# Performance work log

Measured on AMD Instinct MI355X. Metric: run time of the kernel, lower is better.

The kernel has to match this reference:

```python
import jax, jax.numpy as jnp
import numpy as np

N, E, G = 100000, 1600000, 64
IN, H, OUT = 128, 64, 16  # hidden/2 = 32
SLOPE = 0.01


def setup_inputs() -> dict:
    key = jax.random.key(0)
    ks = jax.random.split(key, 7)
    features = jax.random.normal(ks[0], (N, IN), dtype=jnp.float32)
    src = jax.random.randint(ks[1], (E,), 0, N)
    dst = jax.random.randint(ks[2], (E,), 0, N)
    graph_ids = jnp.sort(jax.random.randint(ks[3], (N,), 0, G))
    # kaiming-uniform-ish fan_in init, bias=False everywhere
    W1 = jax.random.uniform(ks[4], (IN, H), jnp.float32, -1.0, 1.0) * np.sqrt(3.0 / IN)
    W2 = jax.random.uniform(ks[5], (H, H // 2), jnp.float32, -1.0, 1.0) * np.sqrt(3.0 / H)
    Wc = jax.random.uniform(ks[6], (H // 2, OUT), jnp.float32, -1.0, 1.0) * np.sqrt(3.0 / (H // 2))
    return {"features": features, "src": src, "dst": dst, "graph_ids": graph_ids,
            "W1": W1, "W2": W2, "Wc": Wc}


def _graph_conv(x, W, src, dst, n):
    # DGL GraphConv, norm='both', bias=False:
    # out = D_in^{-1/2} A (D_out^{-1/2} x) W   (degrees clamped to >= 1)
    ones = jnp.ones(src.shape[0], dtype=x.dtype)
    outdeg = jnp.clip(jax.ops.segment_sum(ones, src, num_segments=n), 1.0)
    indeg = jnp.clip(jax.ops.segment_sum(ones, dst, num_segments=n), 1.0)
    h = (x * jax.lax.rsqrt(outdeg)[:, None]) @ W  # project first (in_dim > out_dim)
    m = jax.ops.segment_sum(h[src], dst, num_segments=n)  # sparse aggregation
    return m * jax.lax.rsqrt(indeg)[:, None]


def reference(features, src, dst, graph_ids, W1, W2, Wc):
    h = jax.nn.leaky_relu(_graph_conv(features, W1, src, dst, N), SLOPE)
    h = jax.nn.leaky_relu(_graph_conv(h, W2, src, dst, N), SLOPE)
    # dropout is identity at inference
    sums = jax.ops.segment_sum(h, graph_ids, num_segments=G)
    cnts = jnp.clip(jax.ops.segment_sum(jnp.ones((N,), h.dtype), graph_ids, num_segments=G), 1.0)
    mean = sums / cnts[:, None]  # dgl.mean_nodes
    return mean @ Wc  # [G, OUT]
```

## Files before the change

kernel.cpp:

```cpp
#include <hip/hip_runtime.h>

#define NN 100000
#define NE 1600000
#define NG 64
#define D_IN 128
#define D_H 64
#define D_H2 32
#define D_OUT 16
#define SLOPE 0.01f
#define REC 48

#define BSH 9
#define NBK 196
#define NCB 256
#define CHE (NE / NCB)
#define CNT_M (2 * NBK * NCB)

typedef _Float16 half2v __attribute__((ext_vector_type(2)));
typedef _Float16 h8 __attribute__((ext_vector_type(8)));
typedef float f32x4 __attribute__((ext_vector_type(4)));

__global__ __launch_bounds__(256) void p1_count(const int* __restrict__ src,
                                                const int* __restrict__ dst,
                                                int* __restrict__ cnt) {
  __shared__ int hD[NBK], hS[NBK];
  int b = blockIdx.x, t = threadIdx.x;
  for (int i = t; i < NBK; i += 256) { hD[i] = 0; hS[i] = 0; }
  __syncthreads();
  int base = b * CHE;
  for (int i = t; i < CHE; i += 256) {
    atomicAdd(&hD[dst[base + i] >> BSH], 1);
    atomicAdd(&hS[src[base + i] >> BSH], 1);
  }
  __syncthreads();
  for (int i = t; i < NBK; i += 256) {
    cnt[i * NCB + b] = hD[i];
    cnt[(NBK + i) * NCB + b] = hS[i];
  }
}

__global__ __launch_bounds__(256) void s1_reduce(const int* __restrict__ cnt,
                                                 int* __restrict__ part) {
  __shared__ int red[256];
  int b = blockIdx.x, t = threadIdx.x;
  red[t] = cnt[b * 256 + t];
  __syncthreads();
  for (int off = 128; off > 0; off >>= 1) {
    if (t < off) red[t] += red[t + off];
    __syncthreads();
  }
  if (t == 0) part[b] = red[0];
}

__global__ __launch_bounds__(512) void s2_scan(int* __restrict__ part) {
  __shared__ int a[512], b2[512];
  int t = threadIdx.x;
  const int M = CNT_M / 256;
  int v = (t < M) ? part[t] : 0;
  a[t] = v;
  __syncthreads();
  int* cur = a; int* nxt = b2;
  for (int off = 1; off < 512; off <<= 1) {
    int x = cur[t];
    if (t >= off) x += cur[t - off];
    nxt[t] = x;
    __syncthreads();
    int* tmp = cur; cur = nxt; nxt = tmp;
  }
  if (t < M) part[t] = cur[t] - v;
}

__global__ __launch_bounds__(256) void s3_apply(int* __restrict__ cnt,
                                                const int* __restrict__ part) {
  __shared__ int wsum[4];
  int b = blockIdx.x, t = threadIdx.x;
  int gid = b * 256 + t;
  int v0 = cnt[gid];
  int lane = t & 63, w = t >> 6;
  int v = v0;
  for (int off = 1; off < 64; off <<= 1) {
    int u = __shfl_up(v, off);
    if (lane >= off) v += u;
  }
  if (lane == 63) wsum[w] = v;
  __syncthreads();
  int woff = 0;
  for (int i = 0; i < w; ++i) woff += wsum[i];
  cnt[gid] = part[b] + woff + (v - v0);
}

__global__ __launch_bounds__(256) void p2_scatter(const int* __restrict__ src,
                                                  const int* __restrict__ dst,
                                                  const int* __restrict__ cnt,
                                                  uint2* __restrict__ pairs,
                                                  int* __restrict__ srcs) {
  __shared__ int cD[NBK], cS[NBK];
  int b = blockIdx.x, t = threadIdx.x;
  for (int i = t; i < NBK; i += 256) {
    cD[i] = cnt[i * NCB + b];
    cS[i] = cnt[(NBK + i) * NCB + b] - NE;
  }
  __syncthreads();
  int base = b * CHE;
  for (int i = t; i < CHE; i += 256) {
    int s = src[base + i], d = dst[base + i];
    int pd = atomicAdd(&cD[d >> BSH], 1);
    pairs[pd] = make_uint2((unsigned)d, (unsigned)s);
    int ps = atomicAdd(&cS[s >> BSH], 1);
    srcs[ps] = s;
  }
}

__global__ __launch_bounds__(256) void p3_build(const uint2* __restrict__ pairs,
                                                const int* __restrict__ srcs,
                                                const int* __restrict__ cnt,
                                                int* __restrict__ adj,
                                                int* __restrict__ indeg,
                                                int* __restrict__ outdeg) {
  __shared__ int hh[512];
  int bb = blockIdx.x, t = threadIdx.x;
  for (int i = t; i < 512; i += 256) hh[i] = 0;
  __syncthreads();
  if (bb < NBK) {
    int k = bb;
    int lo = cnt[k * NCB];
    int hi = cnt[(k + 1) * NCB];
    for (int i = lo + t; i < hi; i += 256) {
      uint2 e = pairs[i];
      int pos = atomicAdd(&hh[e.x & 511], 1);
      if (pos < REC) adj[(size_t)e.x * REC + pos] = (int)e.y;
    }
    __syncthreads();
    int n0 = k << BSH;
    for (int i = t; i < 512; i += 256) {
      int n = n0 + i;
      if (n < NN) {
        int dg = hh[i];
        indeg[n] = dg;
        int d = min(dg, REC);
        int dr = min((d + 15) & ~15, REC);
        for (int j = d; j < dr; ++j) adj[(size_t)n * REC + j] = NN;
      }
    }
  } else {
    int k = bb - NBK;
    int lo = cnt[(NBK + k) * NCB] - NE;
    int hi = ((k == NBK - 1) ? 2 * NE : cnt[(NBK + k + 1) * NCB]) - NE;
    for (int i = lo + t; i < hi; i += 256) atomicAdd(&hh[srcs[i] & 511], 1);
    __syncthreads();
    int n0 = k << BSH;
    for (int i = t; i < 512; i += 256) {
      int n = n0 + i;
      if (n < NN) outdeg[n] = hh[i];
    }
  }
}

__global__ __launch_bounds__(256) void k_mm1f(const float* __restrict__ X,
                                              const float* __restrict__ W,
                                              const int* __restrict__ odeg,
                                              _Float16* __restrict__ Y) {
  __shared__ _Float16 Wt[64][136];
  int t = threadIdx.x;
  if (blockIdx.x == 0 && t < 64) Y[(size_t)NN * 64 + t] = (_Float16)0.f;
  for (int i = t; i < 128 * 64; i += 256) {
    int k = i >> 6, f = i & 63;
    Wt[f][k] = (_Float16)W[i];
  }
  __syncthreads();
  int lane = t & 63, w = t >> 6;
  int m = lane & 15, q = lane >> 4;
  h8 bf[4][4];
#pragma unroll
  for (int kc = 0; kc < 4; ++kc)
#pragma unroll
    for (int nt = 0; nt < 4; ++nt)
      bf[kc][nt] = *(const h8*)&Wt[nt * 16 + m][kc * 32 + q * 8];

  for (int tile = blockIdx.x * 4 + w; tile < NN / 16; tile += gridDim.x * 4) {
    int n0 = tile * 16;
    const f32x4* Xr = (const f32x4*)(X + (size_t)(n0 + m) * 128);
    h8 af[4];
#pragma unroll
    for (int kc = 0; kc < 4; ++kc) {
      f32x4 x0 = Xr[kc * 8 + q * 2 + 0];
      f32x4 x1 = Xr[kc * 8 + q * 2 + 1];
      h8 a;
      a[0] = (_Float16)x0.x; a[1] = (_Float16)x0.y;
      a[2] = (_Float16)x0.z; a[3] = (_Float16)x0.w;
      a[4] = (_Float16)x1.x; a[5] = (_Float16)x1.y;
      a[6] = (_Float16)x1.z; a[7] = (_Float16)x1.w;
      af[kc] = a;
    }
    f32x4 acc[4] = {{0,0,0,0},{0,0,0,0},{0,0,0,0},{0,0,0,0}};
#pragma unroll
    for (int kc = 0; kc < 4; ++kc)
#pragma unroll
      for (int nt = 0; nt < 4; ++nt)
        acc[nt] = __builtin_amdgcn_mfma_f32_16x16x32_f16(af[kc], bf[kc][nt], acc[nt], 0, 0, 0);
#pragma unroll
    for (int reg = 0; reg < 4; ++reg) {
      int nn = n0 + q * 4 + reg;
      float sc = rsqrtf((float)max(odeg[nn], 1));
#pragma unroll
      for (int nt = 0; nt < 4; ++nt)
        Y[(size_t)nn * 64 + nt * 16 + m] = (_Float16)(acc[nt][reg] * sc);
    }
  }
}

__global__ __launch_bounds__(256) void k_mm2f(const _Float16* __restrict__ Xh,
                                              const float* __restrict__ W,
                                              const int* __restrict__ odeg,
                                              _Float16* __restrict__ Y) {
  __shared__ _Float16 Wt[32][72];
  int t = threadIdx.x;
  if (blockIdx.x == 0 && t < 32) Y[(size_t)NN * 32 + t] = (_Float16)0.f;
  for (int i = t; i < 64 * 32; i += 256) {
    int k = i >> 5, f = i & 31;
    Wt[f][k] = (_Float16)W[i];
  }
  __syncthreads();
  int lane = t & 63, w = t >> 6;
  int m = lane & 15, q = lane >> 4;
  h8 bf[2][2];
#pragma unroll
  for (int kc = 0; kc < 2; ++kc)
#pragma unroll
    for (int nt = 0; nt < 2; ++nt)
      bf[kc][nt] = *(const h8*)&Wt[nt * 16 + m][kc * 32 + q * 8];

  for (int tile = blockIdx.x * 4 + w; tile < NN / 16; tile += gridDim.x * 4) {
    int n0 = tile * 16;
    const h8* Xr = (const h8*)(Xh + (size_t)(n0 + m) * 64);
    h8 af[2];
#pragma unroll
    for (int kc = 0; kc < 2; ++kc) af[kc] = Xr[kc * 4 + q];
    f32x4 acc[2] = {{0,0,0,0},{0,0,0,0}};
#pragma unroll
    for (int kc = 0; kc < 2; ++kc)
#pragma unroll
      for (int nt = 0; nt < 2; ++nt)
        acc[nt] = __builtin_amdgcn_mfma_f32_16x16x32_f16(af[kc], bf[kc][nt], acc[nt], 0, 0, 0);
#pragma unroll
    for (int reg = 0; reg < 4; ++reg) {
      int nn = n0 + q * 4 + reg;
      float sc = rsqrtf((float)max(odeg[nn], 1));
#pragma unroll
      for (int nt = 0; nt < 2; ++nt)
        Y[(size_t)nn * 32 + nt * 16 + m] = (_Float16)(acc[nt][reg] * sc);
    }
  }
}

__global__ __launch_bounds__(256) void k_agg64(const int* __restrict__ adj,
                                               const int* __restrict__ indeg,
                                               const half2v* __restrict__ H2,
                                               half2v* __restrict__ Y2) {
  int lane = threadIdx.x & 31;
  int node = blockIdx.x * 8 + (threadIdx.x >> 5);
  int deg = indeg[node];
  int groups = (min(deg, REC) + 15) >> 4;
  const int4* c4 = (const int4*)(adj + (size_t)node * REC);
  float sx = 0.f, sy = 0.f;
  for (int g = 0; g < groups; ++g) {
    int4 ca = c4[g * 4 + 0], cb = c4[g * 4 + 1];
    int4 cc = c4[g * 4 + 2], cd = c4[g * 4 + 3];
    half2v v0 = H2[(size_t)ca.x * 32 + lane];
    half2v v1 = H2[(size_t)ca.y * 32 + lane];
    half2v v2 = H2[(size_t)ca.z * 32 + lane];
    half2v v3 = H2[(size_t)ca.w * 32 + lane];
    half2v v4 = H2[(size_t)cb.x * 32 + lane];
    half2v v5 = H2[(size_t)cb.y * 32 + lane];
    half2v v6 = H2[(size_t)cb.z * 32 + lane];
    half2v v7 = H2[(size_t)cb.w * 32 + lane];
    half2v v8 = H2[(size_t)cc.x * 32 + lane];
    half2v v9 = H2[(size_t)cc.y * 32 + lane];
    half2v va = H2[(size_t)cc.z * 32 + lane];
    half2v vb = H2[(size_t)cc.w * 32 + lane];
    half2v vc = H2[(size_t)cd.x * 32 + lane];
    half2v vd = H2[(size_t)cd.y * 32 + lane];
    half2v ve = H2[(size_t)cd.z * 32 + lane];
    half2v vf = H2[(size_t)cd.w * 32 + lane];
    sx += (((float)v0.x + (float)v1.x) + ((float)v2.x + (float)v3.x)) +
          (((float)v4.x + (float)v5.x) + ((float)v6.x + (float)v7.x)) +
          (((float)v8.x + (float)v9.x) + ((float)va.x + (float)vb.x)) +
          (((float)vc.x + (float)vd.x) + ((float)ve.x + (float)vf.x));
    sy += (((float)v0.y + (float)v1.y) + ((float)v2.y + (float)v3.y)) +
          (((float)v4.y + (float)v5.y) + ((float)v6.y + (float)v7.y)) +
          (((float)v8.y + (float)v9.y) + ((float)va.y + (float)vb.y)) +
          (((float)vc.y + (float)vd.y) + ((float)ve.y + (float)vf.y));
  }
  float sc = rsqrtf((float)max(deg, 1));
  sx *= sc; sy *= sc;
  half2v o = {(_Float16)((sx > 0.f) ? sx : SLOPE * sx),
              (_Float16)((sy > 0.f) ? sy : SLOPE * sy)};
  Y2[(size_t)node * 32 + lane] = o;
}

__global__ __launch_bounds__(256) void k_agg32(const int* __restrict__ adj,
                                               const int* __restrict__ indeg,
                                               const half2v* __restrict__ H2,
                                               half2v* __restrict__ Y2) {
  int lane = threadIdx.x & 15;
  int node = blockIdx.x * 16 + (threadIdx.x >> 4);
  int deg = indeg[node];
  int groups = (min(deg, REC) + 15) >> 4;
  const int4* c4 = (const int4*)(adj + (size_t)node * REC);
  float sx = 0.f, sy = 0.f;
  for (int g = 0; g < groups; ++g) {
    int4 ca = c4[g * 4 + 0], cb = c4[g * 4 + 1];
    int4 cc = c4[g * 4 + 2], cd = c4[g * 4 + 3];
    half2v v0 = H2[(size_t)ca.x * 16 + lane];
    half2v v1 = H2[(size_t)ca.y * 16 + lane];
    half2v v2 = H2[(size_t)ca.z * 16 + lane];
    half2v v3 = H2[(size_t)ca.w * 16 + lane];
    half2v v4 = H2[(size_t)cb.x * 16 + lane];
    half2v v5 = H2[(size_t)cb.y * 16 + lane];
    half2v v6 = H2[(size_t)cb.z * 16 + lane];
    half2v v7 = H2[(size_t)cb.w * 16 + lane];
    half2v v8 = H2[(size_t)cc.x * 16 + lane];
    half2v v9 = H2[(size_t)cc.y * 16 + lane];
    half2v va = H2[(size_t)cc.z * 16 + lane];
    half2v vb = H2[(size_t)cc.w * 16 + lane];
    half2v vc = H2[(size_t)cd.x * 16 + lane];
    half2v vd = H2[(size_t)cd.y * 16 + lane];
    half2v ve = H2[(size_t)cd.z * 16 + lane];
    half2v vf = H2[(size_t)cd.w * 16 + lane];
    sx += (((float)v0.x + (float)v1.x) + ((float)v2.x + (float)v3.x)) +
          (((float)v4.x + (float)v5.x) + ((float)v6.x + (float)v7.x)) +
          (((float)v8.x + (float)v9.x) + ((float)va.x + (float)vb.x)) +
          (((float)vc.x + (float)vd.x) + ((float)ve.x + (float)vf.x));
    sy += (((float)v0.y + (float)v1.y) + ((float)v2.y + (float)v3.y)) +
          (((float)v4.y + (float)v5.y) + ((float)v6.y + (float)v7.y)) +
          (((float)v8.y + (float)v9.y) + ((float)va.y + (float)vb.y)) +
          (((float)vc.y + (float)vd.y) + ((float)ve.y + (float)vf.y));
  }
  float sc = rsqrtf((float)max(deg, 1));
  sx *= sc; sy *= sc;
  half2v o = {(_Float16)((sx > 0.f) ? sx : SLOPE * sx),
              (_Float16)((sy > 0.f) ? sy : SLOPE * sy)};
  Y2[(size_t)node * 16 + lane] = o;
}

__global__ void k_bounds(const int* __restrict__ gid, int* __restrict__ bounds) {
  int n = blockIdx.x * 256 + threadIdx.x;
  if (n < NN) {
    int g = gid[n];
    int gp = (n == 0) ? -1 : gid[n - 1];
    for (int j = gp + 1; j <= g; ++j) bounds[j] = n;
    if (n == NN - 1)
      for (int j = g + 1; j <= NG; ++j) bounds[j] = NN;
  }
}

__global__ __launch_bounds__(256) void k_poolout(const half2v* __restrict__ H2,
                                                 const int* __restrict__ bounds,
                                                 const float* __restrict__ Wc,
                                                 float* __restrict__ out) {
  __shared__ float red[16][33];
  __shared__ float mean[D_H2];
  int g = blockIdx.x, t = threadIdx.x;
  int start = bounds[g], end = bounds[g + 1];
  int c2 = t & 15, r = t >> 4;
  float sx = 0.f, sy = 0.f;
  for (int n = start + r; n < end; n += 16) {
    half2v v = H2[(size_t)n * 16 + c2];
    sx += (float)v.x;
    sy += (float)v.y;
  }
  red[r][c2 * 2] = sx;
  red[r][c2 * 2 + 1] = sy;
  __syncthreads();
  if (r < 8) { red[r][c2 * 2] += red[r + 8][c2 * 2]; red[r][c2 * 2 + 1] += red[r + 8][c2 * 2 + 1]; }
  __syncthreads();
  if (r < 4) { red[r][c2 * 2] += red[r + 4][c2 * 2]; red[r][c2 * 2 + 1] += red[r + 4][c2 * 2 + 1]; }
  __syncthreads();
  if (r < 2) { red[r][c2 * 2] += red[r + 2][c2 * 2]; red[r][c2 * 2 + 1] += red[r + 2][c2 * 2 + 1]; }
  __syncthreads();
  if (r == 0) {
    float inv = 1.0f / (float)max(end - start, 1);
    mean[c2 * 2] = (red[0][c2 * 2] + red[1][c2 * 2]) * inv;
    mean[c2 * 2 + 1] = (red[0][c2 * 2 + 1] + red[1][c2 * 2 + 1]) * inv;
  }
  __syncthreads();
  if (t < D_OUT) {
    float acc = 0.f;
#pragma unroll
    for (int cc = 0; cc < D_H2; ++cc) acc += mean[cc] * Wc[cc * D_OUT + t];
    out[g * D_OUT + t] = acc;
  }
}

extern "C" void kernel_launch(void* const* d_in, const int* in_sizes, int n_in,
                              void* d_out, int out_size, void* d_ws, size_t ws_size,
                              hipStream_t stream) {
  const float* X  = (const float*)d_in[0];
  const int*   src = (const int*)d_in[1];
  const int*   dst = (const int*)d_in[2];
  const int*   gid = (const int*)d_in[3];
  const float* W1 = (const float*)d_in[4];
  const float* W2 = (const float*)d_in[5];
  const float* Wc = (const float*)d_in[6];
  float* out = (float*)d_out;

  char* p = (char*)d_ws;
  auto alloc = [&](size_t bytes) {
    char* q = p;
    p += (bytes + 255) & ~(size_t)255;
    return q;
  };
  int*      outdeg = (int*)alloc(NN * 4);
  int*      indeg  = (int*)alloc(NN * 4);
  int*      bounds = (int*)alloc((NG + 1) * 4);
  int*      cnt    = (int*)alloc((CNT_M + 1) * 4);
  int*      part   = (int*)alloc((CNT_M / 256) * 4);
  uint2*    pairs  = (uint2*)alloc((size_t)NE * 8);
  int*      srcs   = (int*)alloc((size_t)NE * 4);
  int*      adj    = (int*)alloc((size_t)NN * REC * 4);
  _Float16* bufA   = (_Float16*)alloc((size_t)(NN + 1) * 64 * 2);
  _Float16* bufB   = (_Float16*)alloc((size_t)(NN + 1) * 64 * 2);

  p1_count<<<NCB, 256, 0, stream>>>(src, dst, cnt);
  s1_reduce<<<CNT_M / 256, 256, 0, stream>>>(cnt, part);
  s2_scan<<<1, 512, 0, stream>>>(part);
  s3_apply<<<CNT_M / 256, 256, 0, stream>>>(cnt, part);
  p2_scatter<<<NCB, 256, 0, stream>>>(src, dst, cnt, pairs, srcs);
  p3_build<<<2 * NBK, 256, 0, stream>>>(pairs, srcs, cnt, adj, indeg, outdeg);
  k_bounds<<<(NN + 255) / 256, 256, 0, stream>>>(gid, bounds);

  k_mm1f<<<782, 256, 0, stream>>>(X, W1, outdeg, bufA);
  k_agg64<<<NN / 8, 256, 0, stream>>>(adj, indeg, (const half2v*)bufA, (half2v*)bufB);

  k_mm2f<<<782, 256, 0, stream>>>(bufB, W2, outdeg, bufA);
  k_agg32<<<NN / 16, 256, 0, stream>>>(adj, indeg, (const half2v*)bufA, (half2v*)bufB);

  k_poolout<<<NG, 256, 0, stream>>>((const half2v*)bufB, bounds, Wc, out);
}
```

Before: 254.5 us.

## Pack CSR build intermediates into 32-bit/16-bit words and vectorize edge reads

The edge-bucketing pipeline now writes each dst-sorted edge as one 32-bit word (a 9-bit local dst plus a 17-bit src) instead of an 8-byte pair. The src-sorted list is stored as 16-bit local indices instead of 32-bit ints, which cuts scatter and rebuild memory traffic. The chunk count changes from 256 to 250 so each chunk divides by 4 and edges can be read as int4. The count array is padded to a multiple of 256 with a zeroed tail. The two projection kernels are launched with twice as many blocks; the unchanged kernel bodies must handle that grid correctly.

```diff
diff --git a/kernel.cpp b/kernel.cpp
--- a/kernel.cpp
+++ b/kernel.cpp
@@ -12,9 +12,10 @@
 
 #define BSH 9
 #define NBK 196
-#define NCB 256
+#define NCB 250
 #define CHE (NE / NCB)
 #define CNT_M (2 * NBK * NCB)
+#define CNT_R 98048
 
 typedef _Float16 half2v __attribute__((ext_vector_type(2)));
 typedef _Float16 h8 __attribute__((ext_vector_type(8)));
@@ -25,12 +26,17 @@
                                                 int* __restrict__ cnt) {
   __shared__ int hD[NBK], hS[NBK];
   int b = blockIdx.x, t = threadIdx.x;
+  if (b == 0 && t < CNT_R - CNT_M) cnt[CNT_M + t] = 0;
   for (int i = t; i < NBK; i += 256) { hD[i] = 0; hS[i] = 0; }
   __syncthreads();
-  int base = b * CHE;
-  for (int i = t; i < CHE; i += 256) {
-    atomicAdd(&hD[dst[base + i] >> BSH], 1);
-    atomicAdd(&hS[src[base + i] >> BSH], 1);
+  const int4* s4 = (const int4*)(src + b * CHE);
+  const int4* d4 = (const int4*)(dst + b * CHE);
+  for (int i = t; i < CHE / 4; i += 256) {
+    int4 s = s4[i], d = d4[i];
+    atomicAdd(&hD[d.x >> BSH], 1); atomicAdd(&hD[d.y >> BSH], 1);
+    atomicAdd(&hD[d.z >> BSH], 1); atomicAdd(&hD[d.w >> BSH], 1);
+    atomicAdd(&hS[s.x >> BSH], 1); atomicAdd(&hS[s.y >> BSH], 1);
+    atomicAdd(&hS[s.z >> BSH], 1); atomicAdd(&hS[s.w >> BSH], 1);
   }
   __syncthreads();
   for (int i = t; i < NBK; i += 256) {
@@ -55,7 +61,7 @@
 __global__ __launch_bounds__(512) void s2_scan(int* __restrict__ part) {
   __shared__ int a[512], b2[512];
   int t = threadIdx.x;
-  const int M = CNT_M / 256;
+  const int M = CNT_R / 256;
   int v = (t < M) ? part[t] : 0;
   a[t] = v;
   __syncthreads();
@@ -92,8 +98,8 @@
 __global__ __launch_bounds__(256) void p2_scatter(const int* __restrict__ src,
                                                   const int* __restrict__ dst,
                                                   const int* __restrict__ cnt,
-                                                  uint2* __restrict__ pairs,
-                                                  int* __restrict__ srcs) {
+                                                  unsigned* __restrict__ pk,
+                                                  unsigned short* __restrict__ srcs16) {
   __shared__ int cD[NBK], cS[NBK];
   int b = blockIdx.x, t = threadIdx.x;
   for (int i = t; i < NBK; i += 256) {
@@ -101,18 +107,24 @@
     cS[i] = cnt[(NBK + i) * NCB + b] - NE;
   }
   __syncthreads();
-  int base = b * CHE;
-  for (int i = t; i < CHE; i += 256) {
-    int s = src[base + i], d = dst[base + i];
-    int pd = atomicAdd(&cD[d >> BSH], 1);
-    pairs[pd] = make_uint2((unsigned)d, (unsigned)s);
-    int ps = atomicAdd(&cS[s >> BSH], 1);
-    srcs[ps] = s;
-  }
-}
-
-__global__ __launch_bounds__(256) void p3_build(const uint2* __restrict__ pairs,
-                                                const int* __restrict__ srcs,
+  const int4* s4 = (const int4*)(src + b * CHE);
+  const int4* d4 = (const int4*)(dst + b * CHE);
+  for (int i = t; i < CHE / 4; i += 256) {
+    int4 s = s4[i], d = d4[i];
+#pragma unroll
+    for (int j = 0; j < 4; ++j) {
+      int ss = (j == 0) ? s.x : (j == 1) ? s.y : (j == 2) ? s.z : s.w;
+      int dd = (j == 0) ? d.x : (j == 1) ? d.y : (j == 2) ? d.z : d.w;
+      int pd = atomicAdd(&cD[dd >> BSH], 1);
+      pk[pd] = ((unsigned)(dd & 511) << 17) | (unsigned)ss;
+      int ps = atomicAdd(&cS[ss >> BSH], 1);
+      srcs16[ps] = (unsigned short)(ss & 511);
+    }
+  }
+}
+
+__global__ __launch_bounds__(256) void p3_build(const unsigned* __restrict__ pk,
+                                                const unsigned short* __restrict__ srcs16,
                                                 const int* __restrict__ cnt,
                                                 int* __restrict__ adj,
                                                 int* __restrict__ indeg,
@@ -123,15 +135,16 @@
   __syncthreads();
   if (bb < NBK) {
     int k = bb;
+    int n0 = k << BSH;
     int lo = cnt[k * NCB];
     int hi = cnt[(k + 1) * NCB];
     for (int i = lo + t; i < hi; i += 256) {
-      uint2 e = pairs[i];
-      int pos = atomicAdd(&hh[e.x & 511], 1);
-      if (pos < REC) adj[(size_t)e.x * REC + pos] = (int)e.y;
+      unsigned v = pk[i];
+      int local = v >> 17;
+      int pos = atomicAdd(&hh[local], 1);
+      if (pos < REC) adj[(size_t)(n0 + local) * REC + pos] = (int)(v & 0x1FFFF);
     }
     __syncthreads();
-    int n0 = k << BSH;
     for (int i = t; i < 512; i += 256) {
       int n = n0 + i;
       if (n < NN) {
@@ -146,7 +159,7 @@
     int k = bb - NBK;
     int lo = cnt[(NBK + k) * NCB] - NE;
     int hi = ((k == NBK - 1) ? 2 * NE : cnt[(NBK + k + 1) * NCB]) - NE;
-    for (int i = lo + t; i < hi; i += 256) atomicAdd(&hh[srcs[i] & 511], 1);
+    for (int i = lo + t; i < hi; i += 256) atomicAdd(&hh[srcs16[i]], 1);
     __syncthreads();
     int n0 = k << BSH;
     for (int i = t; i < 512; i += 256) {
@@ -410,29 +423,29 @@
     p += (bytes + 255) & ~(size_t)255;
     return q;
   };
-  int*      outdeg = (int*)alloc(NN * 4);
-  int*      indeg  = (int*)alloc(NN * 4);
-  int*      bounds = (int*)alloc((NG + 1) * 4);
-  int*      cnt    = (int*)alloc((CNT_M + 1) * 4);
-  int*      part   = (int*)alloc((CNT_M / 256) * 4);
-  uint2*    pairs  = (uint2*)alloc((size_t)NE * 8);
-  int*      srcs   = (int*)alloc((size_t)NE * 4);
-  int*      adj    = (int*)alloc((size_t)NN * REC * 4);
-  _Float16* bufA   = (_Float16*)alloc((size_t)(NN + 1) * 64 * 2);
-  _Float16* bufB   = (_Float16*)alloc((size_t)(NN + 1) * 64 * 2);
+  int*            outdeg = (int*)alloc(NN * 4);
+  int*            indeg  = (int*)alloc(NN * 4);
+  int*            bounds = (int*)alloc((NG + 1) * 4);
+  int*            cnt    = (int*)alloc((CNT_R + 256) * 4);
+  int*            part   = (int*)alloc((CNT_R / 256) * 4);
+  unsigned*       pk     = (unsigned*)alloc((size_t)NE * 4);
+  unsigned short* srcs16 = (unsigned short*)alloc((size_t)NE * 2);
+  int*            adj    = (int*)alloc((size_t)NN * REC * 4);
+  _Float16*       bufA   = (_Float16*)alloc((size_t)(NN + 1) * 64 * 2);
+  _Float16*       bufB   = (_Float16*)alloc((size_t)(NN + 1) * 64 * 2);
 
   p1_count<<<NCB, 256, 0, stream>>>(src, dst, cnt);
-  s1_reduce<<<CNT_M / 256, 256, 0, stream>>>(cnt, part);
+  s1_reduce<<<CNT_R / 256, 256, 0, stream>>>(cnt, part);
   s2_scan<<<1, 512, 0, stream>>>(part);
-  s3_apply<<<CNT_M / 256, 256, 0, stream>>>(cnt, part);
-  p2_scatter<<<NCB, 256, 0, stream>>>(src, dst, cnt, pairs, srcs);
-  p3_build<<<2 * NBK, 256, 0, stream>>>(pairs, srcs, cnt, adj, indeg, outdeg);
+  s3_apply<<<CNT_R / 256, 256, 0, stream>>>(cnt, part);
+  p2_scatter<<<NCB, 256, 0, stream>>>(src, dst, cnt, pk, srcs16);
+  p3_build<<<2 * NBK, 256, 0, stream>>>(pk, srcs16, cnt, adj, indeg, outdeg);
   k_bounds<<<(NN + 255) / 256, 256, 0, stream>>>(gid, bounds);
 
-  k_mm1f<<<782, 256, 0, stream>>>(X, W1, outdeg, bufA);
+  k_mm1f<<<1563, 256, 0, stream>>>(X, W1, outdeg, bufA);
   k_agg64<<<NN / 8, 256, 0, stream>>>(adj, indeg, (const half2v*)bufA, (half2v*)bufB);
 
-  k_mm2f<<<782, 256, 0, stream>>>(bufB, W2, outdeg, bufA);
+  k_mm2f<<<1563, 256, 0, stream>>>(bufB, W2, outdeg, bufA);
   k_agg32<<<NN / 16, 256, 0, stream>>>(adj, indeg, (const half2v*)bufA, (half2v*)bufB);
 
   k_poolout<<<NG, 256, 0, stream>>>((const half2v*)bufB, bounds, Wc, out);
```

Result: faster. 245.0 us (-3.7%).
